# Performance work log

Measured on AMD Instinct MI355X. Metric: run time of the kernel, lower is better.

## Reference

```python
import jax, jax.numpy as jnp
import numpy as np

N_NODES = 50000
N_EDGES = 1600000
N_GRAPHS = 512
IN_DIM = 64
HID = 128
OUT_DIM = 10


def setup_inputs() -> dict:
    key = jax.random.key(0)
    ks = jax.random.split(key, 12)
    x = jax.random.normal(ks[0], (N_NODES, IN_DIM), dtype=jnp.float32)
    edge_index = jax.random.randint(ks[1], (2, N_EDGES), 0, N_NODES, dtype=jnp.int64)
    batch = jnp.sort(jax.random.randint(ks[2], (N_NODES,), 0, N_GRAPHS, dtype=jnp.int64))
    edge_attr = jax.random.uniform(ks[3], (N_EDGES,), dtype=jnp.float32)
    # glorot-ish init for weights
    def lin(k, fan_in, fan_out):
        s = (6.0 / (fan_in + fan_out)) ** 0.5
        return jax.random.uniform(k, (fan_in, fan_out), minval=-s, maxval=s, dtype=jnp.float32)
    return {
        "x": x, "edge_index": edge_index, "batch": batch, "edge_attr": edge_attr,
        "W1": lin(ks[4], IN_DIM, HID), "b1": jnp.zeros((HID,), jnp.float32),
        "W2": lin(ks[5], HID, HID), "b2": jnp.zeros((HID,), jnp.float32),
        "Wm1": lin(ks[6], HID, HID), "bm1": jnp.zeros((HID,), jnp.float32),
        "Wm2": lin(ks[7], HID, OUT_DIM), "bm2": jnp.zeros((OUT_DIM,), jnp.float32),
    }


def _gcn_conv(x, edge_index, edge_weight, W, b, num_nodes):
    """PyG GCNConv: add self-loops, symmetric norm with edge weights, x@W, scatter-add, +bias."""
    loop = jnp.arange(num_nodes, dtype=edge_index.dtype)
    src = jnp.concatenate([edge_index[0], loop])
    dst = jnp.concatenate([edge_index[1], loop])
    ew = jnp.concatenate([edge_weight, jnp.ones((num_nodes,), edge_weight.dtype)])
    deg = jax.ops.segment_sum(ew, dst, num_segments=num_nodes)  # [N]
    dinv = jnp.where(deg > 0, jax.lax.rsqrt(jnp.where(deg > 0, deg, 1.0)), 0.0)
    norm = dinv[src] * ew * dinv[dst]  # [E+N]
    h = x @ W  # [N, F_out]
    msg = h[src] * norm[:, None]  # gather + scale
    out = jax.ops.segment_sum(msg, dst, num_segments=num_nodes)
    return out + b


def reference(x, edge_index, batch, edge_attr, W1, b1, W2, b2, Wm1, bm1, Wm2, bm2):
    n = x.shape[0]
    h = _gcn_conv(x, edge_index, edge_attr, W1, b1, n)
    h = jax.nn.relu(h)  # dropout = identity in eval mode
    h = _gcn_conv(h, edge_index, edge_attr, W2, b2, n)
    h = jax.nn.relu(h)
    pooled = jax.ops.segment_sum(h, batch, num_segments=N_GRAPHS)  # global_add_pool
    z = jax.nn.relu(pooled @ Wm1 + bm1)
    return z @ Wm2 + bm2  # [num_graphs, out_dim]
```

## Files before the change

### kernel.cpp

```cpp
#include <hip/hip_runtime.h>
#include <hip/hip_bf16.h>
#include <hip/hip_fp16.h>
#include <cstdint>

#define HIDC 128
#define FIXSCALE 4194304.0f
#define FIXINV   (1.0f / 4194304.0f)
#define MAXDEG 80

#define BKT_SHIFT 7
#define BKT_NODES 128
#define BKT_CAP   4608
#define BIN_TILE  4096
#define BIN_THREADS 512

typedef _Float16 half8 __attribute__((ext_vector_type(8)));
typedef float float4v __attribute__((ext_vector_type(4)));

__global__ __launch_bounds__(256) void prep_kernel(
        const float* __restrict__ W1, const float* __restrict__ W2,
        _Float16* __restrict__ W1t, _Float16* __restrict__ W2t,
        unsigned int* __restrict__ tails, int nbkt) {
    int i = blockIdx.x * 256 + threadIdx.x;
    if (i < 16384) { int k = i >> 7, n = i & 127; W2t[n * 128 + k] = (_Float16)W2[i]; }
    if (i < 8192)  { int k = i >> 7, n = i & 127; W1t[n * 64 + k]  = (_Float16)W1[i]; }
    if (i < nbkt) tails[i] = 0u;
}

__global__ __launch_bounds__(BIN_THREADS) void bin_kernel(
        const int* __restrict__ ei, const float* __restrict__ ea,
        unsigned int* __restrict__ buck_lo, unsigned char* __restrict__ buck_dl,
        unsigned int* __restrict__ tails, int E, int nbkt) {
    __shared__ unsigned long long rec[BIN_TILE];
    __shared__ unsigned int cnt[BIN_THREADS];
    __shared__ unsigned int startx[BIN_THREADS];
    __shared__ unsigned int cur[BIN_THREADS];
    __shared__ unsigned int gbase[BIN_THREADS];
    __shared__ unsigned int wtot[BIN_THREADS / 64];
    int t = threadIdx.x;
    int base = blockIdx.x * BIN_TILE;
    int total = E - base; if (total > BIN_TILE) total = BIN_TILE;

    cnt[t] = 0;
    __syncthreads();

    unsigned int lo[8], dv[8];
#pragma unroll
    for (int j = 0; j < 8; ++j) {
        int e = base + j * BIN_THREADS + t;
        if (e < E) {
            int s = ei[e]; int d = ei[E + e]; float w = ea[e];
            lo[j] = (unsigned int)s |
                    ((unsigned int)__half_as_ushort(__float2half_rn(w)) << 16);
            dv[j] = (unsigned int)d;
            atomicAdd(&cnt[dv[j] >> BKT_SHIFT], 1u);
        } else dv[j] = 0xffffffffu;
    }
    __syncthreads();

    unsigned int c = cnt[t];
    unsigned int sc = c;
#pragma unroll
    for (int off = 1; off < 64; off <<= 1) {
        unsigned int v = __shfl_up(sc, off);
        if ((t & 63) >= off) sc += v;
    }
    if ((t & 63) == 63) wtot[t >> 6] = sc;
    __syncthreads();
    unsigned int wbase = 0;
    int w = t >> 6;
    for (int i = 0; i < w; ++i) wbase += wtot[i];
    unsigned int excl = sc + wbase - c;
    startx[t] = excl;
    cur[t] = excl;
    if (t < nbkt) gbase[t] = atomicAdd(&tails[t], c);
    __syncthreads();

#pragma unroll
    for (int j = 0; j < 8; ++j) {
        if (dv[j] != 0xffffffffu) {
            unsigned int p = atomicAdd(&cur[dv[j] >> BKT_SHIFT], 1u);
            rec[p] = ((unsigned long long)dv[j] << 32) | (unsigned long long)lo[j];
        }
    }
    __syncthreads();

    for (int i = t; i < total; i += BIN_THREADS) {
        unsigned long long r = rec[i];
        unsigned int hi = (unsigned int)(r >> 32);
        unsigned int b = hi >> BKT_SHIFT;
        unsigned int idx = gbase[b] + ((unsigned int)i - startx[b]);
        if (idx < BKT_CAP) {
            buck_lo[b * BKT_CAP + idx] = (unsigned int)r;
            buck_dl[b * BKT_CAP + idx] = (unsigned char)(hi & (BKT_NODES - 1));
        }
    }
}

__global__ __launch_bounds__(256) void fill_kernel(
        const unsigned int* __restrict__ buck_lo,
        const unsigned char* __restrict__ buck_dl,
        const unsigned int* __restrict__ tails,
        const float* __restrict__ x,
        unsigned long long* __restrict__ degcnt,
        unsigned int* __restrict__ padcsr,
        _Float16* __restrict__ xt, int n_nodes) {
    __shared__ unsigned long long deg[BKT_NODES];
    __shared__ float sdinv[BKT_NODES];
    int b = blockIdx.x, t = threadIdx.x;
    if (t < BKT_NODES) deg[t] = 0ull;
    __syncthreads();
    int cnt_b = (int)tails[b]; if (cnt_b > BKT_CAP) cnt_b = BKT_CAP;
    unsigned int boff = (unsigned int)b * BKT_CAP;
    int nodeBase = b << BKT_SHIFT;
    for (int i = t; i < cnt_b; i += 256) {
        unsigned int lo = buck_lo[boff + i];
        unsigned int dl = buck_dl[boff + i];
        float w = __half2float(__ushort_as_half((unsigned short)(lo >> 16)));
        unsigned int fx = (unsigned int)(w * FIXSCALE + 0.5f);
        unsigned long long old =
            atomicAdd(&deg[dl], (1ull << 32) | (unsigned long long)fx);
        unsigned int rank = (unsigned int)(old >> 32);
        if (rank < MAXDEG)
            padcsr[(size_t)(nodeBase + dl) * MAXDEG + rank] = lo;
    }
    __syncthreads();
    if (t < BKT_NODES) {
        unsigned long long dv = deg[t];
        sdinv[t] = rsqrtf(1.0f + (float)(unsigned int)(dv & 0xffffffffull) * FIXINV);
        int node = nodeBase + t;
        if (node < n_nodes) degcnt[node] = dv;
    }
    __syncthreads();
    int d = t & 63, nl = t >> 6;
    for (int nn = nl; nn < BKT_NODES; nn += 4) {
        int node = nodeBase + nn;
        if (node < n_nodes)
            xt[(size_t)node * 64 + d] = (_Float16)(x[(size_t)node * 64 + d] * sdinv[nn]);
    }
}

__global__ __launch_bounds__(256) void agg0_kernel(
        const _Float16* __restrict__ xt,
        const unsigned long long* __restrict__ degcnt,
        const unsigned int* __restrict__ padcsr,
        _Float16* __restrict__ g, int n_nodes) {
    int wave = threadIdx.x >> 6, lane = threadIdx.x & 63;
    int node = blockIdx.x * 4 + wave;
    if (node >= n_nodes) return;
    int half = lane >> 5, li = lane & 31;
    unsigned long long v = degcnt[node];
    int cnt = (int)(v >> 32); if (cnt > MAXDEG) cnt = MAXDEG;
    float di = rsqrtf(1.0f + (float)(unsigned int)(v & 0xffffffffull) * FIXINV);
    const unsigned int* row = padcsr + (size_t)node * MAXDEG;
    const __half2* X = (const __half2*)xt;
    float a0 = 0.f, a1 = 0.f;
    int e = 0;
    for (; e + 32 <= cnt; e += 32) {
        unsigned int p[16];
#pragma unroll
        for (int j = 0; j < 16; ++j) p[j] = row[e + 2 * j + half];
        __half2 vv[16];
#pragma unroll
        for (int j = 0; j < 16; ++j)
            vv[j] = X[(p[j] & 0xffffu) * 32u + (unsigned)li];
#pragma unroll
        for (int j = 0; j < 16; ++j) {
            float c = __half2float(__ushort_as_half((unsigned short)(p[j] >> 16)));
            float2 f = __half22float2(vv[j]);
            a0 = fmaf(c, f.x, a0); a1 = fmaf(c, f.y, a1);
        }
    }
    if (e < cnt) {
        int rem = cnt - e;
        unsigned int p[16]; bool m[16];
#pragma unroll
        for (int j = 0; j < 16; ++j) {
            int idx = 2 * j + half;
            m[j] = idx < rem;
            p[j] = m[j] ? row[e + idx] : 0u;
        }
        __half2 vv[16];
#pragma unroll
        for (int j = 0; j < 16; ++j)
            vv[j] = X[(p[j] & 0xffffu) * 32u + (unsigned)li];
#pragma unroll
        for (int j = 0; j < 16; ++j) {
            float c = m[j] ? __half2float(__ushort_as_half((unsigned short)(p[j] >> 16))) : 0.f;
            float2 f = __half22float2(vv[j]);
            a0 = fmaf(c, f.x, a0); a1 = fmaf(c, f.y, a1);
        }
    }
    if (half == 0) {
        float2 f = __half22float2(X[(unsigned)node * 32u + (unsigned)li]);
        a0 += f.x; a1 += f.y;
    }
    a0 += __shfl_xor(a0, 32);
    a1 += __shfl_xor(a1, 32);
    if (half == 0)
        *((__half2*)g + (unsigned)node * 32u + li) = __floats2half2_rn(di * a0, di * a1);
}

__global__ __launch_bounds__(256) void gemm1_mfma_kernel(
        const _Float16* __restrict__ G,
        const _Float16* __restrict__ W1t,
        const float* __restrict__ b1,
        const unsigned long long* __restrict__ degcnt,
        __half* __restrict__ out, int n_nodes) {
    int wave = threadIdx.x >> 6, lane = threadIdx.x & 63;
    int nodeBase = (blockIdx.x * 4 + wave) * 16;
    if (nodeBase >= n_nodes) return;
    int mrow = lane & 15, quad = lane >> 4;

    int anode = nodeBase + mrow; if (anode >= n_nodes) anode = n_nodes - 1;
    const _Float16* Arow = G + (size_t)anode * 64 + quad * 8;
    half8 a[2];
    a[0] = *(const half8*)(Arow);
    a[1] = *(const half8*)(Arow + 32);

    float4v acc[8];
#pragma unroll
    for (int nt = 0; nt < 8; ++nt) acc[nt] = (float4v)(0.f);
#pragma unroll
    for (int nt = 0; nt < 8; ++nt) {
        const _Float16* Brow = W1t + (size_t)(nt * 16 + mrow) * 64 + quad * 8;
#pragma unroll
        for (int q = 0; q < 2; ++q) {
            half8 b = *(const half8*)(Brow + q * 32);
            acc[nt] = __builtin_amdgcn_mfma_f32_16x16x32_f16(a[q], b, acc[nt], 0, 0, 0);
        }
    }
#pragma unroll
    for (int r = 0; r < 4; ++r) {
        int node = nodeBase + quad * 4 + r;
        if (node < n_nodes) {
            unsigned long long v = degcnt[node];
            float di = rsqrtf(1.0f + (float)(unsigned int)(v & 0xffffffffull) * FIXINV);
#pragma unroll
            for (int nt = 0; nt < 8; ++nt) {
                int col = nt * 16 + mrow;
                float val = fmaxf(acc[nt][r] + b1[col], 0.f) * di;
                out[(size_t)node * 128 + col] = __float2half(val);
            }
        }
    }
}

__global__ __launch_bounds__(256) void agg2_kernel(const __half* __restrict__ h,
                                                   const unsigned long long* __restrict__ degcnt,
                                                   const unsigned int* __restrict__ padcsr,
                                                   __half* __restrict__ out, int n_nodes) {
    int wave = threadIdx.x >> 6;
    int lane = threadIdx.x & 63;
    int node = blockIdx.x * 4 + wave;
    if (node >= n_nodes) return;
    unsigned long long v = degcnt[node];
    int cnt = (int)(v >> 32);
    if (cnt > MAXDEG) cnt = MAXDEG;
    float di = rsqrtf(1.0f + (float)(unsigned int)(v & 0xffffffffull) * FIXINV);
    const unsigned int* row = padcsr + (size_t)node * MAXDEG;
    float a0 = 0.f, a1 = 0.f;
    int e = 0;
    for (; e + 16 <= cnt; e += 16) {
        unsigned int p[16];
#pragma unroll
        for (int j = 0; j < 16; ++j) p[j] = row[e + j];
        __half2 vv[16];
#pragma unroll
        for (int j = 0; j < 16; ++j)
            vv[j] = *(reinterpret_cast<const __half2*>(h + (p[j] & 0xffffu) * HIDC) + lane);
#pragma unroll
        for (int j = 0; j < 16; ++j) {
            float c = __half2float(__ushort_as_half((unsigned short)(p[j] >> 16)));
            float2 f = __half22float2(vv[j]);
            a0 = fmaf(c, f.x, a0); a1 = fmaf(c, f.y, a1);
        }
    }
    for (; e + 4 <= cnt; e += 4) {
        unsigned int p[4];
#pragma unroll
        for (int j = 0; j < 4; ++j) p[j] = row[e + j];
        __half2 vv[4];
#pragma unroll
        for (int j = 0; j < 4; ++j)
            vv[j] = *(reinterpret_cast<const __half2*>(h + (p[j] & 0xffffu) * HIDC) + lane);
#pragma unroll
        for (int j = 0; j < 4; ++j) {
            float c = __half2float(__ushort_as_half((unsigned short)(p[j] >> 16)));
            float2 f = __half22float2(vv[j]);
            a0 = fmaf(c, f.x, a0); a1 = fmaf(c, f.y, a1);
        }
    }
    for (; e < cnt; ++e) {
        unsigned int p = row[e];
        float c = __half2float(__ushort_as_half((unsigned short)(p >> 16)));
        float2 f = __half22float2(*(reinterpret_cast<const __half2*>(h + (p & 0xffffu) * HIDC) + lane));
        a0 = fmaf(c, f.x, a0); a1 = fmaf(c, f.y, a1);
    }
    float2 fn = __half22float2(*(reinterpret_cast<const __half2*>(h + (size_t)node * HIDC) + lane));
    a0 = di * (a0 + fn.x);
    a1 = di * (a1 + fn.y);
    *(reinterpret_cast<__half2*>(out + (size_t)node * HIDC) + lane) =
        __floats2half2_rn(a0, a1);
}

__global__ __launch_bounds__(256) void gemm2_mfma_kernel(
        const __half* __restrict__ A,
        const _Float16* __restrict__ W2t,
        const float* __restrict__ b2,
        __half* __restrict__ out, int n_nodes) {
    int wave = threadIdx.x >> 6, lane = threadIdx.x & 63;
    int nodeBase = (blockIdx.x * 4 + wave) * 16;
    if (nodeBase >= n_nodes) return;
    int mrow = lane & 15, quad = lane >> 4;

    int anode = nodeBase + mrow; if (anode >= n_nodes) anode = n_nodes - 1;
    const _Float16* Arow = (const _Float16*)A + (size_t)anode * 128 + quad * 8;
    half8 a[4];
#pragma unroll
    for (int q = 0; q < 4; ++q) a[q] = *(const half8*)(Arow + q * 32);

    float4v acc[8];
#pragma unroll
    for (int nt = 0; nt < 8; ++nt) acc[nt] = (float4v)(0.f);
#pragma unroll
    for (int nt = 0; nt < 8; ++nt) {
        const _Float16* Brow = W2t + (size_t)(nt * 16 + mrow) * 128 + quad * 8;
#pragma unroll
        for (int q = 0; q < 4; ++q) {
            half8 b = *(const half8*)(Brow + q * 32);
            acc[nt] = __builtin_amdgcn_mfma_f32_16x16x32_f16(a[q], b, acc[nt], 0, 0, 0);
        }
    }
#pragma unroll
    for (int r = 0; r < 4; ++r) {
        int node = nodeBase + quad * 4 + r;
        if (node < n_nodes) {
#pragma unroll
            for (int nt = 0; nt < 8; ++nt) {
                int col = nt * 16 + mrow;
                float val = fmaxf(acc[nt][r] + b2[col], 0.f);
                out[(size_t)node * 128 + col] = __float2half(val);
            }
        }
    }
}

__global__ __launch_bounds__(256) void pool_mlp_kernel(const __half* __restrict__ h,
                                                       const int* __restrict__ batch,
                                                       const float* __restrict__ Wm1,
                                                       const float* __restrict__ bm1,
                                                       const float* __restrict__ Wm2,
                                                       const float* __restrict__ bm2,
                                                       float* __restrict__ out,
                                                       int n_nodes, int out_dim) {
    int g = blockIdx.x;
    int t = threadIdx.x;
    __shared__ int sb[2];
    __shared__ float row2[256];
    __shared__ float row[128];
    __shared__ float zl[128];
    if (t < 2) {
        int target = g + t;
        int lo = 0, hi = n_nodes;
        while (lo < hi) { int mid = (lo + hi) >> 1; if (batch[mid] < target) lo = mid + 1; else hi = mid; }
        sb[t] = lo;
    }
    __syncthreads();
    int beg = sb[0], end = sb[1];
    int dim = t & 127, sub = t >> 7;
    float p = 0.f;
    for (int i = beg + sub; i < end; i += 2)
        p += __half2float(h[(size_t)i * 128 + dim]);
    row2[t] = p;
    __syncthreads();
    if (t < 128) row[t] = row2[t] + row2[t + 128];
    __syncthreads();
    if (t < 128) {
        float acc = bm1[t];
#pragma unroll 8
        for (int k = 0; k < 128; ++k) acc += row[k] * Wm1[k * 128 + t];
        zl[t] = fmaxf(acc, 0.f);
    }
    __syncthreads();
    if (t < out_dim) {
        float o = bm2[t];
#pragma unroll 8
        for (int k = 0; k < 128; ++k) o += zl[k] * Wm2[k * out_dim + t];
        out[g * out_dim + t] = o;
    }
}

extern "C" void kernel_launch(void* const* d_in, const int* in_sizes, int n_in,
                              void* d_out, int out_size, void* d_ws, size_t ws_size,
                              hipStream_t stream) {
    const float* x   = (const float*)d_in[0];
    const int*   ei  = (const int*)d_in[1];
    const int*   bat = (const int*)d_in[2];
    const float* ea  = (const float*)d_in[3];
    const float* W1  = (const float*)d_in[4];
    const float* b1  = (const float*)d_in[5];
    const float* W2  = (const float*)d_in[6];
    const float* b2  = (const float*)d_in[7];
    const float* Wm1 = (const float*)d_in[8];
    const float* bm1 = (const float*)d_in[9];
    const float* Wm2 = (const float*)d_in[10];
    const float* bm2 = (const float*)d_in[11];
    float* out = (float*)d_out;

    const int N = in_sizes[2];
    const int E = in_sizes[1] / 2;
    const int N_GRAPHS = 512;
    const int OUT_DIM = out_size / N_GRAPHS;

    char* ws = (char*)d_ws;
    size_t off = 0;
    auto alloc = [&](size_t bytes) { char* p = ws + off; off += (bytes + 255) & ~size_t(255); return p; };
    char* regB = alloc((size_t)N * HIDC * 2);
    char* regC = alloc((size_t)N * HIDC * 2);
    char* regA = alloc((size_t)N * MAXDEG * 4);
    unsigned long long* degcnt = (unsigned long long*)alloc((size_t)N * 8);
    _Float16* W2t = (_Float16*)alloc(128 * 128 * 2);
    _Float16* W1t = (_Float16*)alloc(128 * 64 * 2);
    unsigned int* tails = (unsigned int*)alloc(BIN_THREADS * 4);

    int nbkt = (N + BKT_NODES - 1) >> BKT_SHIFT;
    unsigned int*  buck_lo = (unsigned int*)regB;
    unsigned char* buck_dl = (unsigned char*)(regB + (size_t)nbkt * BKT_CAP * 4);
    __half*    htld = (__half*)regB;
    _Float16*  xt   = (_Float16*)regC;
    _Float16*  gbuf = (_Float16*)(regC + (size_t)N * 64 * 2);
    __half*    ubuf = (__half*)regC;
    unsigned int* padcsr = (unsigned int*)regA;
    __half*    zbuf = (__half*)regA;

    prep_kernel<<<64, 256, 0, stream>>>(W1, W2, W1t, W2t, tails, nbkt);
    int binBlocks = (E + BIN_TILE - 1) / BIN_TILE;
    bin_kernel<<<binBlocks, BIN_THREADS, 0, stream>>>(ei, ea, buck_lo, buck_dl, tails, E, nbkt);
    fill_kernel<<<nbkt, 256, 0, stream>>>(buck_lo, buck_dl, tails, x, degcnt, padcsr, xt, N);
    agg0_kernel<<<(N + 3) / 4, 256, 0, stream>>>(xt, degcnt, padcsr, gbuf, N);
    gemm1_mfma_kernel<<<(N + 63) / 64, 256, 0, stream>>>(gbuf, W1t, b1, degcnt, htld, N);
    agg2_kernel<<<(N + 3) / 4, 256, 0, stream>>>(htld, degcnt, padcsr, ubuf, N);
    gemm2_mfma_kernel<<<(N + 63) / 64, 256, 0, stream>>>(ubuf, W2t, b2, zbuf, N);
    pool_mlp_kernel<<<N_GRAPHS, 256, 0, stream>>>(zbuf, bat, Wm1, bm1, Wm2, bm2, out, N, OUT_DIM);
}
```

Baseline: 278.3 us.

## Use 16-byte row gathers with multi-edge lane groups in both aggregation kernels

Both aggregation kernels now have each lane load 8 halfs (16 bytes) of a neighbor row instead of one half2, so one wave handles several edges at once: 8 in agg0, 4 in agg2. The per-lane partial sums are then combined with xor shuffles. Padded CSR rows are zero-filled up to a multiple of 8 in the bucket kernel, which removes masked tail handling. The aim is fewer, wider gather instructions and more memory-level parallelism per wave, at the cost of extra shuffle reductions and writes for the padding.

Measured after the change: 263.2 us (median of 2 runs). 1.06x faster.

```diff
diff --git a/kernel.cpp b/kernel.cpp
--- a/kernel.cpp
+++ b/kernel.cpp
@@ -129,7 +129,13 @@
         unsigned long long dv = deg[t];
         sdinv[t] = rsqrtf(1.0f + (float)(unsigned int)(dv & 0xffffffffull) * FIXINV);
         int node = nodeBase + t;
-        if (node < n_nodes) degcnt[node] = dv;
+        if (node < n_nodes) {
+            degcnt[node] = dv;
+            int cw = (int)(dv >> 32); if (cw > MAXDEG) cw = MAXDEG;
+            int cp = (cw + 7) & ~7;
+            for (int r = cw; r < cp; ++r)
+                padcsr[(size_t)node * MAXDEG + r] = 0u;
+        }
     }
     __syncthreads();
     int d = t & 63, nl = t >> 6;
@@ -148,57 +154,164 @@
     int wave = threadIdx.x >> 6, lane = threadIdx.x & 63;
     int node = blockIdx.x * 4 + wave;
     if (node >= n_nodes) return;
-    int half = lane >> 5, li = lane & 31;
+    int qd = lane >> 3, li = lane & 7;
     unsigned long long v = degcnt[node];
     int cnt = (int)(v >> 32); if (cnt > MAXDEG) cnt = MAXDEG;
+    int cntp = (cnt + 7) & ~7;
     float di = rsqrtf(1.0f + (float)(unsigned int)(v & 0xffffffffull) * FIXINV);
     const unsigned int* row = padcsr + (size_t)node * MAXDEG;
-    const __half2* X = (const __half2*)xt;
-    float a0 = 0.f, a1 = 0.f;
+    unsigned base_li = (unsigned)(li * 8);
+    float acc[8];
+#pragma unroll
+    for (int k = 0; k < 8; ++k) acc[k] = 0.f;
     int e = 0;
-    for (; e + 32 <= cnt; e += 32) {
-        unsigned int p[16];
-#pragma unroll
-        for (int j = 0; j < 16; ++j) p[j] = row[e + 2 * j + half];
-        __half2 vv[16];
-#pragma unroll
-        for (int j = 0; j < 16; ++j)
-            vv[j] = X[(p[j] & 0xffffu) * 32u + (unsigned)li];
-#pragma unroll
-        for (int j = 0; j < 16; ++j) {
-            float c = __half2float(__ushort_as_half((unsigned short)(p[j] >> 16)));
-            float2 f = __half22float2(vv[j]);
-            a0 = fmaf(c, f.x, a0); a1 = fmaf(c, f.y, a1);
-        }
-    }
-    if (e < cnt) {
-        int rem = cnt - e;
-        unsigned int p[16]; bool m[16];
-#pragma unroll
-        for (int j = 0; j < 16; ++j) {
-            int idx = 2 * j + half;
-            m[j] = idx < rem;
-            p[j] = m[j] ? row[e + idx] : 0u;
-        }
-        __half2 vv[16];
-#pragma unroll
-        for (int j = 0; j < 16; ++j)
-            vv[j] = X[(p[j] & 0xffffu) * 32u + (unsigned)li];
-#pragma unroll
-        for (int j = 0; j < 16; ++j) {
-            float c = m[j] ? __half2float(__ushort_as_half((unsigned short)(p[j] >> 16))) : 0.f;
-            float2 f = __half22float2(vv[j]);
-            a0 = fmaf(c, f.x, a0); a1 = fmaf(c, f.y, a1);
-        }
-    }
-    if (half == 0) {
-        float2 f = __half22float2(X[(unsigned)node * 32u + (unsigned)li]);
-        a0 += f.x; a1 += f.y;
-    }
-    a0 += __shfl_xor(a0, 32);
-    a1 += __shfl_xor(a1, 32);
-    if (half == 0)
-        *((__half2*)g + (unsigned)node * 32u + li) = __floats2half2_rn(di * a0, di * a1);
+    for (; e + 32 <= cntp; e += 32) {
+        unsigned int p[4];
+#pragma unroll
+        for (int j = 0; j < 4; ++j) p[j] = row[e + 8 * j + qd];
+        uint4 vv[4];
+#pragma unroll
+        for (int j = 0; j < 4; ++j)
+            vv[j] = *reinterpret_cast<const uint4*>(
+                xt + (p[j] & 0xffffu) * 64u + base_li);
+#pragma unroll
+        for (int j = 0; j < 4; ++j) {
+            __half ch = __ushort_as_half((unsigned short)(p[j] >> 16));
+            float cf = __half2float(ch);
+            const __half2* hp = reinterpret_cast<const __half2*>(&vv[j]);
+#pragma unroll
+            for (int k = 0; k < 4; ++k) {
+                float2 f = __half22float2(hp[k]);
+                acc[2 * k]     = fmaf(cf, f.x, acc[2 * k]);
+                acc[2 * k + 1] = fmaf(cf, f.y, acc[2 * k + 1]);
+            }
+        }
+    }
+    for (; e < cntp; e += 8) {
+        unsigned int p = row[e + qd];
+        uint4 vv = *reinterpret_cast<const uint4*>(
+            xt + (p & 0xffffu) * 64u + base_li);
+        __half ch = __ushort_as_half((unsigned short)(p >> 16));
+        float cf = __half2float(ch);
+        const __half2* hp = reinterpret_cast<const __half2*>(&vv);
+#pragma unroll
+        for (int k = 0; k < 4; ++k) {
+            float2 f = __half22float2(hp[k]);
+            acc[2 * k]     = fmaf(cf, f.x, acc[2 * k]);
+            acc[2 * k + 1] = fmaf(cf, f.y, acc[2 * k + 1]);
+        }
+    }
+#pragma unroll
+    for (int k = 0; k < 8; ++k) {
+        acc[k] += __shfl_xor(acc[k], 8);
+        acc[k] += __shfl_xor(acc[k], 16);
+        acc[k] += __shfl_xor(acc[k], 32);
+    }
+    if (qd == 0) {
+        uint4 sv = *reinterpret_cast<const uint4*>(
+            xt + (unsigned)node * 64u + base_li);
+        const __half2* sp = reinterpret_cast<const __half2*>(&sv);
+        __half2 o[4];
+#pragma unroll
+        for (int k = 0; k < 4; ++k) {
+            float2 f = __half22float2(sp[k]);
+            o[k] = __floats2half2_rn(di * (acc[2 * k] + f.x),
+                                     di * (acc[2 * k + 1] + f.y));
+        }
+        uint4 st;
+        st.x = *reinterpret_cast<unsigned int*>(&o[0]);
+        st.y = *reinterpret_cast<unsigned int*>(&o[1]);
+        st.z = *reinterpret_cast<unsigned int*>(&o[2]);
+        st.w = *reinterpret_cast<unsigned int*>(&o[3]);
+        *reinterpret_cast<uint4*>(g + (size_t)node * 64 + base_li) = st;
+    }
+}
+
+__global__ __launch_bounds__(256) void agg2_kernel(const __half* __restrict__ h,
+                                                   const unsigned long long* __restrict__ degcnt,
+                                                   const unsigned int* __restrict__ padcsr,
+                                                   __half* __restrict__ out, int n_nodes) {
+    int wave = threadIdx.x >> 6, lane = threadIdx.x & 63;
+    int node = blockIdx.x * 4 + wave;
+    if (node >= n_nodes) return;
+    int qd = lane >> 4, li = lane & 15;
+    unsigned long long v = degcnt[node];
+    int cnt = (int)(v >> 32); if (cnt > MAXDEG) cnt = MAXDEG;
+    int cntp = (cnt + 7) & ~7;
+    float di = rsqrtf(1.0f + (float)(unsigned int)(v & 0xffffffffull) * FIXINV);
+    const unsigned int* row = padcsr + (size_t)node * MAXDEG;
+    unsigned base_li = (unsigned)(li * 8);
+    float acc[8];
+#pragma unroll
+    for (int k = 0; k < 8; ++k) acc[k] = 0.f;
+    int e = 0;
+    for (; e + 32 <= cntp; e += 32) {
+        unsigned int p[8];
+#pragma unroll
+        for (int j = 0; j < 8; ++j) p[j] = row[e + 4 * j + qd];
+        uint4 vv[8];
+#pragma unroll
+        for (int j = 0; j < 8; ++j)
+            vv[j] = *reinterpret_cast<const uint4*>(
+                h + (p[j] & 0xffffu) * 128u + base_li);
+#pragma unroll
+        for (int j = 0; j < 8; ++j) {
+            __half ch = __ushort_as_half((unsigned short)(p[j] >> 16));
+            float cf = __half2float(ch);
+            const __half2* hp = reinterpret_cast<const __half2*>(&vv[j]);
+#pragma unroll
+            for (int k = 0; k < 4; ++k) {
+                float2 f = __half22float2(hp[k]);
+                acc[2 * k]     = fmaf(cf, f.x, acc[2 * k]);
+                acc[2 * k + 1] = fmaf(cf, f.y, acc[2 * k + 1]);
+            }
+        }
+    }
+    for (; e < cntp; e += 8) {
+        unsigned int p[2];
+#pragma unroll
+        for (int j = 0; j < 2; ++j) p[j] = row[e + 4 * j + qd];
+        uint4 vv[2];
+#pragma unroll
+        for (int j = 0; j < 2; ++j)
+            vv[j] = *reinterpret_cast<const uint4*>(
+                h + (p[j] & 0xffffu) * 128u + base_li);
+#pragma unroll
+        for (int j = 0; j < 2; ++j) {
+            __half ch = __ushort_as_half((unsigned short)(p[j] >> 16));
+            float cf = __half2float(ch);
+            const __half2* hp = reinterpret_cast<const __half2*>(&vv[j]);
+#pragma unroll
+            for (int k = 0; k < 4; ++k) {
+                float2 f = __half22float2(hp[k]);
+                acc[2 * k]     = fmaf(cf, f.x, acc[2 * k]);
+                acc[2 * k + 1] = fmaf(cf, f.y, acc[2 * k + 1]);
+            }
+        }
+    }
+#pragma unroll
+    for (int k = 0; k < 8; ++k) {
+        acc[k] += __shfl_xor(acc[k], 16);
+        acc[k] += __shfl_xor(acc[k], 32);
+    }
+    if (qd == 0) {
+        uint4 sv = *reinterpret_cast<const uint4*>(
+            h + (unsigned)node * 128u + base_li);
+        const __half2* sp = reinterpret_cast<const __half2*>(&sv);
+        __half2 o[4];
+#pragma unroll
+        for (int k = 0; k < 4; ++k) {
+            float2 f = __half22float2(sp[k]);
+            o[k] = __floats2half2_rn(di * (acc[2 * k] + f.x),
+                                     di * (acc[2 * k + 1] + f.y));
+        }
+        uint4 st;
+        st.x = *reinterpret_cast<unsigned int*>(&o[0]);
+        st.y = *reinterpret_cast<unsigned int*>(&o[1]);
+        st.z = *reinterpret_cast<unsigned int*>(&o[2]);
+        st.w = *reinterpret_cast<unsigned int*>(&o[3]);
+        *reinterpret_cast<uint4*>(out + (size_t)node * 128 + base_li) = st;
+    }
 }
 
 __global__ __launch_bounds__(256) void gemm1_mfma_kernel(
@@ -244,64 +357,6 @@
             }
         }
     }
-}
-
-__global__ __launch_bounds__(256) void agg2_kernel(const __half* __restrict__ h,
-                                                   const unsigned long long* __restrict__ degcnt,
-                                                   const unsigned int* __restrict__ padcsr,
-                                                   __half* __restrict__ out, int n_nodes) {
-    int wave = threadIdx.x >> 6;
-    int lane = threadIdx.x & 63;
-    int node = blockIdx.x * 4 + wave;
-    if (node >= n_nodes) return;
-    unsigned long long v = degcnt[node];
-    int cnt = (int)(v >> 32);
-    if (cnt > MAXDEG) cnt = MAXDEG;
-    float di = rsqrtf(1.0f + (float)(unsigned int)(v & 0xffffffffull) * FIXINV);
-    const unsigned int* row = padcsr + (size_t)node * MAXDEG;
-    float a0 = 0.f, a1 = 0.f;
-    int e = 0;
-    for (; e + 16 <= cnt; e += 16) {
-        unsigned int p[16];
-#pragma unroll
-        for (int j = 0; j < 16; ++j) p[j] = row[e + j];
-        __half2 vv[16];
-#pragma unroll
-        for (int j = 0; j < 16; ++j)
-            vv[j] = *(reinterpret_cast<const __half2*>(h + (p[j] & 0xffffu) * HIDC) + lane);
-#pragma unroll
-        for (int j = 0; j < 16; ++j) {
-            float c = __half2float(__ushort_as_half((unsigned short)(p[j] >> 16)));
-            float2 f = __half22float2(vv[j]);
-            a0 = fmaf(c, f.x, a0); a1 = fmaf(c, f.y, a1);
-        }
-    }
-    for (; e + 4 <= cnt; e += 4) {
-        unsigned int p[4];
-#pragma unroll
-        for (int j = 0; j < 4; ++j) p[j] = row[e + j];
-        __half2 vv[4];
-#pragma unroll
-        for (int j = 0; j < 4; ++j)
-            vv[j] = *(reinterpret_cast<const __half2*>(h + (p[j] & 0xffffu) * HIDC) + lane);
-#pragma unroll
-        for (int j = 0; j < 4; ++j) {
-            float c = __half2float(__ushort_as_half((unsigned short)(p[j] >> 16)));
-            float2 f = __half22float2(vv[j]);
-            a0 = fmaf(c, f.x, a0); a1 = fmaf(c, f.y, a1);
-        }
-    }
-    for (; e < cnt; ++e) {
-        unsigned int p = row[e];
-        float c = __half2float(__ushort_as_half((unsigned short)(p >> 16)));
-        float2 f = __half22float2(*(reinterpret_cast<const __half2*>(h + (p & 0xffffu) * HIDC) + lane));
-        a0 = fmaf(c, f.x, a0); a1 = fmaf(c, f.y, a1);
-    }
-    float2 fn = __half22float2(*(reinterpret_cast<const __half2*>(h + (size_t)node * HIDC) + lane));
-    a0 = di * (a0 + fn.x);
-    a1 = di * (a1 + fn.y);
-    *(reinterpret_cast<__half2*>(out + (size_t)node * HIDC) + lane) =
-        __floats2half2_rn(a0, a1);
 }
 
 __global__ __launch_bounds__(256) void gemm2_mfma_kernel(
```
